# Optimization experiments

Measured on AMD Instinct MI355X. Metric: run time of the kernel, lower is better.

Reference implementation:

```python
import jax, jax.numpy as jnp
import numpy as np

EPS = 1e-12
BETA = 0.25

def normalise(x, axis=-1):
    return x * jax.lax.rsqrt(jnp.mean(x * x, axis=axis, keepdims=True) + EPS)

def setup_inputs() -> dict:
    key = jax.random.key(0)
    ks = jax.random.split(key, 4)
    N, F, D, C = 8192, 512, 64, 8192
    return {
        "z": jax.random.normal(ks[0], (N, F), dtype=jnp.float32),
        "W_in": jax.random.normal(ks[1], (F, D), dtype=jnp.float32) * (1.0 / np.sqrt(F)),
        "b_in": jnp.zeros((D,), dtype=jnp.float32),
        "codebook": jax.random.normal(ks[2], (C, D), dtype=jnp.float32),
        "W_out": jax.random.normal(ks[3], (D, F), dtype=jnp.float32) * (1.0 / np.sqrt(D)),
        "b_out": jnp.zeros((F,), dtype=jnp.float32),
    }

def reference(z, W_in, b_in, codebook, W_out, b_out):
    sg = jax.lax.stop_gradient
    # input projection: [N, F] -> [N, D]
    zp = z @ W_in + b_in
    zn = normalise(zp)                  # [N, D]
    cn = normalise(codebook)            # [C, D]
    # squared euclidean distance via matmul expansion (same math as
    # sum((z[:,None]-c[None])**2, -1), avoids [N,C,D] materialization)
    z_sq = jnp.sum(zn * zn, axis=-1, keepdims=True)          # [N, 1]
    c_sq = jnp.sum(cn * cn, axis=-1)[None, :]                # [1, C]
    distance = z_sq + c_sq - 2.0 * (zn @ cn.T)               # [N, C]
    idxes = jnp.argmin(distance, axis=-1)                    # [N]
    codes = normalise(codebook[idxes], axis=-1)               # [N, D]
    loss = BETA * jnp.mean((sg(zn) - codes) ** 2) + jnp.mean((zn - sg(codes)) ** 2)
    codes = zn + sg(codes - zn)                               # straight-through
    out = codes @ W_out + b_out                               # [N, F]
    return (out, loss, idxes)
```

## Files before the change

kernel.cpp:

```cpp
#include <hip/hip_runtime.h>
#include <hip/hip_bf16.h>

#define N_ROWS 8192
#define F_DIM  512
#define D_DIM  64
#define C_CODES 8192

typedef __attribute__((ext_vector_type(8))) short bf16x8;
typedef __attribute__((ext_vector_type(4))) float f32x4;

__device__ __forceinline__ unsigned short rne_bf16(float x) {
  unsigned u = __float_as_uint(x);
  return (unsigned short)((u + 0x7FFFu + ((u >> 16) & 1u)) >> 16);
}
__device__ __forceinline__ float bf16_to_f(unsigned short u) {
  return __uint_as_float(((unsigned)u) << 16);
}
__device__ __forceinline__ void limb3(const float* xs, bf16x8& H, bf16x8& M, bf16x8& L) {
  #pragma unroll
  for (int j = 0; j < 8; ++j) {
    float x = xs[j];
    unsigned short h = rne_bf16(x);
    float r1 = x - bf16_to_f(h);
    unsigned short m = rne_bf16(r1);
    float r2 = r1 - bf16_to_f(m);
    unsigned short lo = rne_bf16(r2);
    H[j] = (short)h; M[j] = (short)m; L[j] = (short)lo;
  }
}

typedef __attribute__((address_space(1))) const unsigned char gas_uchar;
typedef __attribute__((address_space(3))) unsigned char las_uchar;
__device__ __forceinline__ void gld_lds16(const void* g, void* l) {
  __builtin_amdgcn_global_load_lds((gas_uchar*)g, (las_uchar*)l, 16, 0, 0);
}

__global__ __launch_bounds__(256) void k_prep(
    const float* __restrict__ W_in, const float* __restrict__ W_out,
    const float* __restrict__ cb,
    unsigned short* __restrict__ win_sw, unsigned short* __restrict__ wout_sw,
    float* __restrict__ cn, unsigned short* __restrict__ cn_sw,
    float* __restrict__ loss_f) {
  const int tid = threadIdx.x, w = tid >> 6, l = tid & 63;
  const int lo = l & 15, hi = l >> 4;
  const int bid = blockIdx.x;
  if (bid == 0 && tid == 0) loss_f[0] = 0.0f;

  if (bid < 16) {
    const int task = bid * 4 + w;
    const int kc = task >> 2, cg = task & 3;
    float xs[8];
    #pragma unroll
    for (int j = 0; j < 8; ++j)
      xs[j] = W_in[(size_t)(kc * 32 + hi * 8 + j) * D_DIM + cg * 16 + lo];
    bf16x8 H, M, L;
    limb3(xs, H, M, L);
    const int fb = (kc * 4 + cg) * 3;
    unsigned short* d0 = win_sw + (size_t)(fb + 0) * 512 + l * 8;
    *(bf16x8*)d0 = H;
    *(bf16x8*)(d0 + 512) = M;
    *(bf16x8*)(d0 + 1024) = L;
  } else if (bid < 32) {
    const int task = (bid - 16) * 4 + w;
    const int cg = task >> 1, c = task & 1;
    float xs[8];
    #pragma unroll
    for (int j = 0; j < 8; ++j)
      xs[j] = W_out[(size_t)(c * 32 + hi * 8 + j) * F_DIM + cg * 16 + lo];
    bf16x8 H, M, L;
    limb3(xs, H, M, L);
    const int fb = (cg * 2 + c) * 3;
    unsigned short* d0 = wout_sw + (size_t)(fb + 0) * 512 + l * 8;
    *(bf16x8*)d0 = H;
    *(bf16x8*)(d0 + 512) = M;
    *(bf16x8*)(d0 + 1024) = L;
  } else {
    const int g = (bid - 32) * 4 + w;
    const int code = g * 16 + lo;
    float xs[2][8];
    float s = 0.0f;
    #pragma unroll
    for (int c = 0; c < 2; ++c) {
      const float* sp = cb + (size_t)code * D_DIM + c * 32 + hi * 8;
      float4 a = *(const float4*)sp, b = *(const float4*)(sp + 4);
      xs[c][0]=a.x; xs[c][1]=a.y; xs[c][2]=a.z; xs[c][3]=a.w;
      xs[c][4]=b.x; xs[c][5]=b.y; xs[c][6]=b.z; xs[c][7]=b.w;
      #pragma unroll
      for (int j = 0; j < 8; ++j) s += xs[c][j] * xs[c][j];
    }
    s += __shfl_xor(s, 16);
    s += __shfl_xor(s, 32);
    float inv = rsqrtf(s * (1.0f / 64.0f) + 1e-12f);
    #pragma unroll
    for (int c = 0; c < 2; ++c) {
      #pragma unroll
      for (int j = 0; j < 8; ++j) xs[c][j] *= inv;
      float* dp = cn + (size_t)code * D_DIM + c * 32 + hi * 8;
      *(float4*)dp = make_float4(xs[c][0], xs[c][1], xs[c][2], xs[c][3]);
      *(float4*)(dp + 4) = make_float4(xs[c][4], xs[c][5], xs[c][6], xs[c][7]);
      bf16x8 H, M, L;
      limb3(xs[c], H, M, L);
      const int fb = (g * 2 + c) * 3;
      unsigned short* d0 = cn_sw + (size_t)(fb + 0) * 512 + l * 8;
      *(bf16x8*)d0 = H;
      *(bf16x8*)(d0 + 512) = M;
      *(bf16x8*)(d0 + 1024) = L;
    }
  }
}

__global__ __launch_bounds__(256) void k_zn(
    const float* __restrict__ z, const unsigned short* __restrict__ w_in_sw,
    const float* __restrict__ b_in, float* __restrict__ zn,
    unsigned short* __restrict__ zn_sw) {
  __shared__ float red[4096];
  __shared__ float t_lds[16 * 65];
  const int tid = threadIdx.x, w = tid >> 6, l = tid & 63;
  const int lo = l & 15, hi = l >> 4;
  const int g = blockIdx.x;
  const int r0 = g * 16;
  const int kcb = w * 4;
  const bf16x8* Bptr = (const bf16x8*)w_in_sw;
  const float* zbase = z + (size_t)(r0 + lo) * F_DIM + hi * 8;

  f32x4 acc[4];
  #pragma unroll
  for (int cg = 0; cg < 4; ++cg) acc[cg] = (f32x4){0.f, 0.f, 0.f, 0.f};

  bf16x8 Bu[12], Bv[12];
  #pragma unroll
  for (int i = 0; i < 12; ++i) Bu[i] = Bptr[((size_t)kcb * 12 + i) * 64 + l];
  float4 za = *(const float4*)(zbase + kcb * 32);
  float4 zb = *(const float4*)(zbase + kcb * 32 + 4);

  #define ZMFMA(BCUR)                                                         \
    {                                                                         \
      float xs[8] = {za.x, za.y, za.z, za.w, zb.x, zb.y, zb.z, zb.w};         \
      bf16x8 Ah, Am, Al;                                                      \
      limb3(xs, Ah, Am, Al);                                                  \
      _Pragma("unroll")                                                       \
      for (int cg = 0; cg < 4; ++cg) {                                        \
        f32x4 t = acc[cg];                                                    \
        t = __builtin_amdgcn_mfma_f32_16x16x32_bf16(Ah, BCUR[cg*3+0], t, 0,0,0); \
        t = __builtin_amdgcn_mfma_f32_16x16x32_bf16(Ah, BCUR[cg*3+1], t, 0,0,0); \
        t = __builtin_amdgcn_mfma_f32_16x16x32_bf16(Am, BCUR[cg*3+0], t, 0,0,0); \
        t = __builtin_amdgcn_mfma_f32_16x16x32_bf16(Ah, BCUR[cg*3+2], t, 0,0,0); \
        t = __builtin_amdgcn_mfma_f32_16x16x32_bf16(Al, BCUR[cg*3+0], t, 0,0,0); \
        t = __builtin_amdgcn_mfma_f32_16x16x32_bf16(Am, BCUR[cg*3+1], t, 0,0,0); \
        acc[cg] = t;                                                          \
      }                                                                       \
    }

  {
    float4 na = *(const float4*)(zbase + (kcb + 1) * 32);
    float4 nb = *(const float4*)(zbase + (kcb + 1) * 32 + 4);
    #pragma unroll
    for (int i = 0; i < 12; ++i) Bv[i] = Bptr[((size_t)(kcb + 1) * 12 + i) * 64 + l];
    ZMFMA(Bu)
    za = na; zb = nb;
  }
  {
    float4 na = *(const float4*)(zbase + (kcb + 2) * 32);
    float4 nb = *(const float4*)(zbase + (kcb + 2) * 32 + 4);
    #pragma unroll
    for (int i = 0; i < 12; ++i) Bu[i] = Bptr[((size_t)(kcb + 2) * 12 + i) * 64 + l];
    ZMFMA(Bv)
    za = na; zb = nb;
  }
  {
    float4 na = *(const float4*)(zbase + (kcb + 3) * 32);
    float4 nb = *(const float4*)(zbase + (kcb + 3) * 32 + 4);
    #pragma unroll
    for (int i = 0; i < 12; ++i) Bv[i] = Bptr[((size_t)(kcb + 3) * 12 + i) * 64 + l];
    ZMFMA(Bu)
    za = na; zb = nb;
  }
  ZMFMA(Bv)
  #undef ZMFMA

  #pragma unroll
  for (int cg = 0; cg < 4; ++cg)
    #pragma unroll
    for (int r = 0; r < 4; ++r)
      red[((w * 4 + cg) * 4 + r) * 64 + l] = acc[cg][r];
  __syncthreads();

  {
    float v[4], s = 0.0f;
    #pragma unroll
    for (int cg = 0; cg < 4; ++cg) {
      float t = b_in[cg * 16 + lo];
      #pragma unroll
      for (int w2 = 0; w2 < 4; ++w2) t += red[((w2 * 4 + cg) * 4 + w) * 64 + l];
      v[cg] = t; s += t * t;
    }
    s += __shfl_xor(s, 1);
    s += __shfl_xor(s, 2);
    s += __shfl_xor(s, 4);
    s += __shfl_xor(s, 8);
    float inv = rsqrtf(s * (1.0f / 64.0f) + 1e-12f);
    #pragma unroll
    for (int cg = 0; cg < 4; ++cg)
      t_lds[(hi * 4 + w) * 65 + cg * 16 + lo] = v[cg] * inv;
  }
  __syncthreads();

  if (w < 2) {
    const int c = w;
    float xs[8];
    #pragma unroll
    for (int j = 0; j < 8; ++j) xs[j] = t_lds[lo * 65 + c * 32 + hi * 8 + j];
    float* dp = zn + (size_t)(r0 + lo) * D_DIM + c * 32 + hi * 8;
    *(float4*)dp = make_float4(xs[0], xs[1], xs[2], xs[3]);
    *(float4*)(dp + 4) = make_float4(xs[4], xs[5], xs[6], xs[7]);
    bf16x8 H, M, L;
    limb3(xs, H, M, L);
    const int fb = (g * 2 + c) * 3;
    unsigned short* d0 = zn_sw + (size_t)(fb + 0) * 512 + l * 8;
    *(bf16x8*)d0 = H;
    *(bf16x8*)(d0 + 512) = M;
    *(bf16x8*)(d0 + 1024) = L;
  }
}

__global__ __launch_bounds__(512) void k_argmax(
    const unsigned short* __restrict__ zn_sw,
    const unsigned short* __restrict__ cn_sw,
    float* __restrict__ pval, int* __restrict__ pidx) {
  __shared__ short smem[2 * 24 * 512];
  const int tid = threadIdx.x;
  const int w = tid >> 6, l = tid & 63;
  const int lo = l & 15, hi = l >> 4;
  const int gA0 = (blockIdx.x * 8 + w) * 2;
  const int gB0 = blockIdx.y * 32;
  const bf16x8* Ab = (const bf16x8*)zn_sw;
  const char* Bbytes = (const char*)cn_sw;

  bf16x8 A0[2][3], A1[2][3];
  #pragma unroll
  for (int c = 0; c < 2; ++c)
    #pragma unroll
    for (int m = 0; m < 3; ++m) {
      A0[c][m] = Ab[(size_t)((gA0 * 2 + c) * 3 + m) * 64 + l];
      A1[c][m] = Ab[(size_t)(((gA0 + 1) * 2 + c) * 3 + m) * 64 + l];
    }

  float bv[8];
  int bi[8];
  #pragma unroll
  for (int i = 0; i < 8; ++i) { bv[i] = -1e30f; bi[i] = 0; }
  int cand = blockIdx.y * 512 + lo;

  #define STAGE(b, s)                                                         \
    {                                                                         \
      const int fb = (gB0 + (s) * 4) * 6 + w * 3;                             \
      _Pragma("unroll")                                                       \
      for (int i = 0; i < 3; ++i)                                             \
        gld_lds16(Bbytes + ((size_t)(fb + i) << 10) + (size_t)l * 16,         \
                  &smem[((b) * 24 + w * 3 + i) * 512]);                       \
    }

  #define MF(A_, B_, C_) __builtin_amdgcn_mfma_f32_16x16x32_bf16(A_, B_, C_, 0, 0, 0)

  #define COMPUTE(LF)                                                         \
    {                                                                         \
      bf16x8 Bf[6];                                                           \
      _Pragma("unroll")                                                       \
      for (int i = 0; i < 6; ++i)                                             \
        Bf[i] = *(const bf16x8*)&smem[((LF) + i) * 512 + l * 8];              \
      f32x4 a0 = {0.f,0.f,0.f,0.f}, a1 = {0.f,0.f,0.f,0.f};                   \
      f32x4 a2 = {0.f,0.f,0.f,0.f}, a3 = {0.f,0.f,0.f,0.f};                   \
      a0 = MF(A0[0][0], Bf[0], a0); a1 = MF(A0[1][0], Bf[3], a1);             \
      a2 = MF(A1[0][0], Bf[0], a2); a3 = MF(A1[1][0], Bf[3], a3);             \
      a0 = MF(A0[0][0], Bf[1], a0); a1 = MF(A0[1][0], Bf[4], a1);             \
      a2 = MF(A1[0][0], Bf[1], a2); a3 = MF(A1[1][0], Bf[4], a3);             \
      a0 = MF(A0[0][1], Bf[0], a0); a1 = MF(A0[1][1], Bf[3], a1);             \
      a2 = MF(A1[0][1], Bf[0], a2); a3 = MF(A1[1][1], Bf[3], a3);             \
      a0 = MF(A0[0][0], Bf[2], a0); a1 = MF(A0[1][0], Bf[5], a1);             \
      a2 = MF(A1[0][0], Bf[2], a2); a3 = MF(A1[1][0], Bf[5], a3);             \
      a0 = MF(A0[0][2], Bf[0], a0); a1 = MF(A0[1][2], Bf[3], a1);             \
      a2 = MF(A1[0][2], Bf[0], a2); a3 = MF(A1[1][2], Bf[3], a3);             \
      a0 = MF(A0[0][1], Bf[1], a0); a1 = MF(A0[1][1], Bf[4], a1);             \
      a2 = MF(A1[0][1], Bf[1], a2); a3 = MF(A1[1][1], Bf[4], a3);             \
      _Pragma("unroll")                                                       \
      for (int r = 0; r < 4; ++r) {                                           \
        float d0 = a0[r] + a1[r];                                             \
        if (d0 > bv[r]) { bv[r] = d0; bi[r] = cand; }                         \
        float d1 = a2[r] + a3[r];                                             \
        if (d1 > bv[4 + r]) { bv[4 + r] = d1; bi[4 + r] = cand; }             \
      }                                                                       \
      cand += 16;                                                             \
    }

  STAGE(0, 0)
  __syncthreads();
  int cur = 0;
  for (int s = 0; s < 8; ++s) {
    if (s < 7) STAGE(cur ^ 1, s + 1)
    COMPUTE(cur * 24 + 0)
    COMPUTE(cur * 24 + 6)
    COMPUTE(cur * 24 + 12)
    COMPUTE(cur * 24 + 18)
    __syncthreads();
    cur ^= 1;
  }
  #undef STAGE
  #undef COMPUTE
  #undef MF

  #pragma unroll
  for (int i = 0; i < 8; ++i) {
    float v = bv[i]; int ix = bi[i];
    #pragma unroll
    for (int m = 1; m < 16; m <<= 1) {
      float ov = __shfl_xor(v, m);
      int oi = __shfl_xor(ix, m);
      if (ov > v || (ov == v && oi < ix)) { v = ov; ix = oi; }
    }
    bv[i] = v; bi[i] = ix;
  }
  if (lo == 0) {
    int off = blockIdx.y * N_ROWS;
    int base0 = gA0 * 16 + hi * 4;
    int base1 = (gA0 + 1) * 16 + hi * 4;
    #pragma unroll
    for (int r = 0; r < 4; ++r) {
      pval[off + base0 + r] = bv[r];     pidx[off + base0 + r] = bi[r];
      pval[off + base1 + r] = bv[4 + r]; pidx[off + base1 + r] = bi[4 + r];
    }
  }
}

__global__ __launch_bounds__(256) void k_out(
    const float* __restrict__ cn, const float* __restrict__ zn,
    const float* __restrict__ pval, const int* __restrict__ pidx,
    const unsigned short* __restrict__ w_out_sw,
    const float* __restrict__ b_out, float* __restrict__ out,
    float* __restrict__ idx_f, float* __restrict__ loss_f) {
  const int tid = threadIdx.x, w = tid >> 6, l = tid & 63;
  const int lo = l & 15, hi = l >> 4;
  const int r0 = blockIdx.x * 16;
  const int row = r0 + lo;

  float v = pval[row];
  int ix = pidx[row];
  #pragma unroll
  for (int q = 1; q < 16; ++q) {
    float vq = pval[q * N_ROWS + row];
    int iq = pidx[q * N_ROWS + row];
    if (vq > v) { v = vq; ix = iq; }
  }
  if (w == 0 && hi == 0) idx_f[row] = (float)ix;

  bf16x8 A[2][3];
  float lp = 0.0f;
  #pragma unroll
  for (int c = 0; c < 2; ++c) {
    const float* cp = cn + (size_t)ix * D_DIM + c * 32 + hi * 8;
    const float* zp = zn + (size_t)row * D_DIM + c * 32 + hi * 8;
    float4 c0 = *(const float4*)cp, c1 = *(const float4*)(cp + 4);
    float4 z0 = *(const float4*)zp, z1 = *(const float4*)(zp + 4);
    float xs[8] = {c0.x, c0.y, c0.z, c0.w, c1.x, c1.y, c1.z, c1.w};
    float zs[8] = {z0.x, z0.y, z0.z, z0.w, z1.x, z1.y, z1.z, z1.w};
    limb3(xs, A[c][0], A[c][1], A[c][2]);
    #pragma unroll
    for (int j = 0; j < 8; ++j) { float d = xs[j] - zs[j]; lp += d * d; }
  }
  if (w == 0) {
    #pragma unroll
    for (int m = 1; m < 64; m <<= 1) lp += __shfl_xor(lp, m);
    if (l == 0) atomicAdd(loss_f, lp * (1.25f / (float)(N_ROWS * D_DIM)));
  }

  const bf16x8* Bptr = (const bf16x8*)w_out_sw;
  const int cgb = w * 8;
  bf16x8 Bu[6], Bv[6];
  #pragma unroll
  for (int i = 0; i < 6; ++i) Bu[i] = Bptr[((size_t)cgb * 6 + i) * 64 + l];

  #define OSTEP(BCUR, BNXT, CG)                                               \
    {                                                                         \
      _Pragma("unroll")                                                       \
      for (int i = 0; i < 6; ++i)                                             \
        BNXT[i] = Bptr[((size_t)((CG) + 1) * 6 + i) * 64 + l];                \
      f32x4 a0 = {0.f,0.f,0.f,0.f}, a1 = {0.f,0.f,0.f,0.f};                   \
      a0 = __builtin_amdgcn_mfma_f32_16x16x32_bf16(A[0][0], BCUR[0], a0, 0,0,0); \
      a1 = __builtin_amdgcn_mfma_f32_16x16x32_bf16(A[1][0], BCUR[3], a1, 0,0,0); \
      a0 = __builtin_amdgcn_mfma_f32_16x16x32_bf16(A[0][0], BCUR[1], a0, 0,0,0); \
      a1 = __builtin_amdgcn_mfma_f32_16x16x32_bf16(A[1][0], BCUR[4], a1, 0,0,0); \
      a0 = __builtin_amdgcn_mfma_f32_16x16x32_bf16(A[0][1], BCUR[0], a0, 0,0,0); \
      a1 = __builtin_amdgcn_mfma_f32_16x16x32_bf16(A[1][1], BCUR[3], a1, 0,0,0); \
      a0 = __builtin_amdgcn_mfma_f32_16x16x32_bf16(A[0][0], BCUR[2], a0, 0,0,0); \
      a1 = __builtin_amdgcn_mfma_f32_16x16x32_bf16(A[1][0], BCUR[5], a1, 0,0,0); \
      a0 = __builtin_amdgcn_mfma_f32_16x16x32_bf16(A[0][2], BCUR[0], a0, 0,0,0); \
      a1 = __builtin_amdgcn_mfma_f32_16x16x32_bf16(A[1][2], BCUR[3], a1, 0,0,0); \
      a0 = __builtin_amdgcn_mfma_f32_16x16x32_bf16(A[0][1], BCUR[1], a0, 0,0,0); \
      a1 = __builtin_amdgcn_mfma_f32_16x16x32_bf16(A[1][1], BCUR[4], a1, 0,0,0); \
      float bb = b_out[(CG) * 16 + lo];                                       \
      _Pragma("unroll")                                                       \
      for (int r = 0; r < 4; ++r)                                             \
        out[(size_t)(r0 + hi * 4 + r) * F_DIM + (CG) * 16 + lo] =             \
            a0[r] + a1[r] + bb;                                               \
    }

  for (int cg = cgb; cg < cgb + 8; cg += 2) {
    OSTEP(Bu, Bv, cg)
    OSTEP(Bv, Bu, cg + 1)
  }
  #undef OSTEP
}

extern "C" void kernel_launch(void* const* d_in, const int* in_sizes, int n_in,
                              void* d_out, int out_size, void* d_ws, size_t ws_size,
                              hipStream_t stream) {
  const float* z        = (const float*)d_in[0];
  const float* W_in     = (const float*)d_in[1];
  const float* b_in     = (const float*)d_in[2];
  const float* codebook = (const float*)d_in[3];
  const float* W_out    = (const float*)d_in[4];
  const float* b_out    = (const float*)d_in[5];

  float* outp   = (float*)d_out;
  float* loss_f = outp + (size_t)N_ROWS * F_DIM;
  float* idx_f  = loss_f + 1;

  float* wsf = (float*)d_ws;
  float* zn_ws = wsf;
  float* cn_ws = wsf + 524288;
  unsigned short* zn_sw = (unsigned short*)(wsf + 1048576);
  unsigned short* cn_sw = (unsigned short*)(wsf + 1835008);
  unsigned short* win_sw  = (unsigned short*)(wsf + 2625536);
  unsigned short* wout_sw = (unsigned short*)(wsf + 2674688);
  float* pval_ws = wsf + 2723840;
  int*   pidx_ws = (int*)(wsf + 2854912);

  hipLaunchKernelGGL(k_prep, dim3(160), dim3(256), 0, stream,
                     W_in, W_out, codebook, win_sw, wout_sw, cn_ws, cn_sw,
                     loss_f);
  hipLaunchKernelGGL(k_zn, dim3(512), dim3(256), 0, stream,
                     z, win_sw, b_in, zn_ws, zn_sw);
  hipLaunchKernelGGL(k_argmax, dim3(32, 16), dim3(512), 0, stream,
                     zn_sw, cn_sw, pval_ws, pidx_ws);
  hipLaunchKernelGGL(k_out, dim3(512), dim3(256), 0, stream,
                     cn_ws, zn_ws, pval_ws, pidx_ws, wout_sw, b_out,
                     outp, idx_f, loss_f);
}
```

Measured before the change: 141.3 us.

## Split argmax over more codebook chunks and merge partials with 64-bit atomicMax

The argmax kernel's codebook split doubles from 16 to 32 chunks, giving twice as many blocks, each running half as many stages. Per-chunk partial results are no longer written to pval/pidx arrays and reduced in k_out. Instead each block packs an order-preserving float key with the inverted index into a 64-bit value and merges it into a per-row best buffer with atomicMax. k_prep zeroes that buffer. This raises parallelism and removes the 16-way partial read in k_out, in exchange for atomic traffic and a shorter pipeline per block.

```diff
diff --git a/kernel.cpp b/kernel.cpp
--- a/kernel.cpp
+++ b/kernel.cpp
@@ -40,11 +40,14 @@
     const float* __restrict__ cb,
     unsigned short* __restrict__ win_sw, unsigned short* __restrict__ wout_sw,
     float* __restrict__ cn, unsigned short* __restrict__ cn_sw,
-    float* __restrict__ loss_f) {
+    float* __restrict__ loss_f, unsigned long long* __restrict__ best) {
   const int tid = threadIdx.x, w = tid >> 6, l = tid & 63;
   const int lo = l & 15, hi = l >> 4;
   const int bid = blockIdx.x;
-  if (bid == 0 && tid == 0) loss_f[0] = 0.0f;
+  if (bid == 0) {
+    if (tid == 0) loss_f[0] = 0.0f;
+    for (int i = tid; i < N_ROWS; i += 256) best[i] = 0ull;
+  }
 
   if (bid < 16) {
     const int task = bid * 4 + w;
@@ -226,13 +229,13 @@
 __global__ __launch_bounds__(512) void k_argmax(
     const unsigned short* __restrict__ zn_sw,
     const unsigned short* __restrict__ cn_sw,
-    float* __restrict__ pval, int* __restrict__ pidx) {
+    unsigned long long* __restrict__ best) {
   __shared__ short smem[2 * 24 * 512];
   const int tid = threadIdx.x;
   const int w = tid >> 6, l = tid & 63;
   const int lo = l & 15, hi = l >> 4;
   const int gA0 = (blockIdx.x * 8 + w) * 2;
-  const int gB0 = blockIdx.y * 32;
+  const int gB0 = blockIdx.y * 16;
   const bf16x8* Ab = (const bf16x8*)zn_sw;
   const char* Bbytes = (const char*)cn_sw;
 
@@ -249,7 +252,7 @@
   int bi[8];
   #pragma unroll
   for (int i = 0; i < 8; ++i) { bv[i] = -1e30f; bi[i] = 0; }
-  int cand = blockIdx.y * 512 + lo;
+  int cand = blockIdx.y * 256 + lo;
 
   #define STAGE(b, s)                                                         \
     {                                                                         \
@@ -295,8 +298,8 @@
   STAGE(0, 0)
   __syncthreads();
   int cur = 0;
-  for (int s = 0; s < 8; ++s) {
-    if (s < 7) STAGE(cur ^ 1, s + 1)
+  for (int s = 0; s < 4; ++s) {
+    if (s < 3) STAGE(cur ^ 1, s + 1)
     COMPUTE(cur * 24 + 0)
     COMPUTE(cur * 24 + 6)
     COMPUTE(cur * 24 + 12)
@@ -320,20 +323,25 @@
     bv[i] = v; bi[i] = ix;
   }
   if (lo == 0) {
-    int off = blockIdx.y * N_ROWS;
-    int base0 = gA0 * 16 + hi * 4;
-    int base1 = (gA0 + 1) * 16 + hi * 4;
+    const int base0 = gA0 * 16 + hi * 4;
+    const int base1 = (gA0 + 1) * 16 + hi * 4;
     #pragma unroll
     for (int r = 0; r < 4; ++r) {
-      pval[off + base0 + r] = bv[r];     pidx[off + base0 + r] = bi[r];
-      pval[off + base1 + r] = bv[4 + r]; pidx[off + base1 + r] = bi[4 + r];
+      unsigned k0 = __float_as_uint(bv[r]);
+      k0 = (k0 & 0x80000000u) ? ~k0 : (k0 | 0x80000000u);
+      atomicMax(&best[base0 + r],
+                ((unsigned long long)k0 << 32) | (unsigned)(~bi[r]));
+      unsigned k1 = __float_as_uint(bv[4 + r]);
+      k1 = (k1 & 0x80000000u) ? ~k1 : (k1 | 0x80000000u);
+      atomicMax(&best[base1 + r],
+                ((unsigned long long)k1 << 32) | (unsigned)(~bi[4 + r]));
     }
   }
 }
 
 __global__ __launch_bounds__(256) void k_out(
     const float* __restrict__ cn, const float* __restrict__ zn,
-    const float* __restrict__ pval, const int* __restrict__ pidx,
+    const unsigned long long* __restrict__ best,
     const unsigned short* __restrict__ w_out_sw,
     const float* __restrict__ b_out, float* __restrict__ out,
     float* __restrict__ idx_f, float* __restrict__ loss_f) {
@@ -342,14 +350,7 @@
   const int r0 = blockIdx.x * 16;
   const int row = r0 + lo;
 
-  float v = pval[row];
-  int ix = pidx[row];
-  #pragma unroll
-  for (int q = 1; q < 16; ++q) {
-    float vq = pval[q * N_ROWS + row];
-    int iq = pidx[q * N_ROWS + row];
-    if (vq > v) { v = vq; ix = iq; }
-  }
+  const int ix = (int)(~(unsigned)best[row]);
   if (w == 0 && hi == 0) idx_f[row] = (float)ix;
 
   bf16x8 A[2][3];
@@ -431,17 +432,16 @@
   unsigned short* cn_sw = (unsigned short*)(wsf + 1835008);
   unsigned short* win_sw  = (unsigned short*)(wsf + 2625536);
   unsigned short* wout_sw = (unsigned short*)(wsf + 2674688);
-  float* pval_ws = wsf + 2723840;
-  int*   pidx_ws = (int*)(wsf + 2854912);
+  unsigned long long* best_ws = (unsigned long long*)(wsf + 2723840);
 
   hipLaunchKernelGGL(k_prep, dim3(160), dim3(256), 0, stream,
                      W_in, W_out, codebook, win_sw, wout_sw, cn_ws, cn_sw,
-                     loss_f);
+                     loss_f, best_ws);
   hipLaunchKernelGGL(k_zn, dim3(512), dim3(256), 0, stream,
                      z, win_sw, b_in, zn_ws, zn_sw);
-  hipLaunchKernelGGL(k_argmax, dim3(32, 16), dim3(512), 0, stream,
-                     zn_sw, cn_sw, pval_ws, pidx_ws);
+  hipLaunchKernelGGL(k_argmax, dim3(32, 32), dim3(512), 0, stream,
+                     zn_sw, cn_sw, best_ws);
   hipLaunchKernelGGL(k_out, dim3(512), dim3(256), 0, stream,
-                     cn_ws, zn_ws, pval_ws, pidx_ws, wout_sw, b_out,
+                     cn_ws, zn_ws, best_ws, wout_sw, b_out,
                      outp, idx_f, loss_f);
 }
```

Result: no change. 139.9 us (-1.0%).
